# Kernel tuning notes

Measured on AMD Instinct MI355X. Metric: run time of the kernel, lower is better.

## Reference

```python
import jax, jax.numpy as jnp
import numpy as np

B, T, D, H = 64, 512, 512, 1024


def setup_inputs() -> dict:
    key = jax.random.key(0)
    k0, k1, k2, k3, k4 = jax.random.split(key, 5)
    s0 = 1.0 / np.sqrt(D + H)   # torch nn.Linear init bound, layer 0
    s1 = 1.0 / np.sqrt(H + H)   # layer 1
    x = jax.random.normal(k0, (B, T, D), jnp.float32)
    W0 = jax.random.uniform(k1, (4 * H, D + H), jnp.float32, -s0, s0)
    b0 = jax.random.uniform(k2, (4 * H,), jnp.float32, -s0, s0)
    W1 = jax.random.uniform(k3, (4 * H, H + H), jnp.float32, -s1, s1)
    b1 = jax.random.uniform(k4, (4 * H,), jnp.float32, -s1, s1)
    return {"x": x, "W0": W0, "b0": b0, "W1": W1, "b1": b1}


def _lstm_layer(x, W, b):
    # x: (B, T, Din); W: (4H, Din+H); b: (4H,)
    hdim = b.shape[0] // 4
    bsz = x.shape[0]
    h0 = jnp.zeros((bsz, hdim), x.dtype)
    c0 = jnp.zeros((bsz, hdim), x.dtype)

    def step(carry, x_t):
        h, c = carry
        z = jnp.concatenate([x_t, h], axis=-1) @ W.T + b  # (B, 4H)
        i, f, o, g = jnp.split(z, 4, axis=-1)             # torch split order i,f,o,g
        c_next = jax.nn.sigmoid(f) * c + jax.nn.sigmoid(i) * jnp.tanh(g)
        h_next = jax.nn.sigmoid(o) * jnp.tanh(c_next)
        return (h_next, c_next), h_next

    (_, _), hs = jax.lax.scan(step, (h0, c0), jnp.swapaxes(x, 0, 1))
    return jnp.swapaxes(hs, 0, 1)  # (B, T, H)


def reference(x, W0, b0, W1, b1):
    y = _lstm_layer(x, W0, b0)
    y = _lstm_layer(y, W1, b1)
    return y  # last layer output sequence (return_all_layers=False)
```

## Files before the change

### kernel.cpp

```cpp
#include <hip/hip_runtime.h>
#include <hip/hip_bf16.h>

typedef __bf16 bf16x8 __attribute__((ext_vector_type(8)));
typedef float  f32x4  __attribute__((ext_vector_type(4)));

#define MFMA16(a, b, c) __builtin_amdgcn_mfma_f32_16x16x32_bf16((a), (b), (c), 0, 0, 0)

static constexpr int Bz = 64, Tz = 512, Dz = 512, Hz = 1024;
static constexpr int NWG0 = 128;
static constexpr int NWGT = 256;
static constexpr int NJ   = 8;

static constexpr int PXL = 512 + 8;
static constexpr int PHL = 1024 + 8;
static constexpr size_t LDS_BYTES = (size_t)(2 * 32 * PXL + 32 * PHL) * 2;

static constexpr size_t N_W0X = 4096ull * 512;
static constexpr size_t N_W0H = 4096ull * 1024;
static constexpr size_t N_W1  = 4096ull * 2048;
static constexpr size_t N_Y0  = 64ull * 512 * 1024;
static constexpr size_t N_X   = 64ull * 512 * 512;
static constexpr size_t OFF_W0XH = 0;
static constexpr size_t OFF_W0XL = OFF_W0XH + N_W0X;
static constexpr size_t OFF_W0H  = OFF_W0XL + N_W0X;
static constexpr size_t OFF_W1   = OFF_W0H  + N_W0H;
static constexpr size_t OFF_Y0   = OFF_W1   + N_W1;
static constexpr size_t FLAGS_BYTE = (((OFF_Y0 + N_Y0) * 2) + 255) & ~(size_t)255;
static constexpr size_t H1S_BYTE   = FLAGS_BYTE + 4096;
static constexpr size_t WS_NEED    = H1S_BYTE + N_Y0 * 2;
static constexpr size_t XHI_BYTE   = H1S_BYTE + N_Y0 * 2;
static constexpr size_t XLO_BYTE   = XHI_BYTE + N_X * 2;
static constexpr size_t WS_NEED_X  = XLO_BYTE + N_X * 2;

static constexpr int STEP_ELEMS = 65536;

__device__ __forceinline__ float sigm(float x) { return 1.0f / (1.0f + __expf(-x)); }

__device__ __forceinline__ void st_agent_u32(void* p, unsigned v)
{ __hip_atomic_store((unsigned*)p, v, __ATOMIC_RELAXED, __HIP_MEMORY_SCOPE_AGENT); }
__device__ __forceinline__ void st_agent_f32(float* p, float v)
{ __hip_atomic_store(p, v, __ATOMIC_RELAXED, __HIP_MEMORY_SCOPE_AGENT); }

extern "C" __global__ void prep_split(const float* __restrict__ x,
                                      const float* __restrict__ W0,
                                      const float* __restrict__ W1,
                                      __bf16* __restrict__ ws,
                                      __bf16* __restrict__ xhi,
                                      __bf16* __restrict__ xlo)
{
    if (blockIdx.x == 0)
        for (int i = threadIdx.x; i < 1024; i += 256)
            ((unsigned*)((char*)ws + FLAGS_BYTE))[i] = 0u;

    __bf16* w0xh = ws + OFF_W0XH;
    __bf16* w0xl = ws + OFF_W0XL;
    __bf16* w0h  = ws + OFF_W0H;
    __bf16* w1c  = ws + OFF_W1;
    const size_t ntot = N_W0X + N_W0H + N_W1;
    const size_t stride = (size_t)gridDim.x * blockDim.x;
    for (size_t idx = (size_t)blockIdx.x * blockDim.x + threadIdx.x;
         idx < ntot; idx += stride) {
        if (idx < N_W0X) {
            size_t r = idx >> 9, c = idx & 511;
            float w = W0[r * 1536 + c];
            __bf16 hi = (__bf16)w;
            w0xh[idx] = hi;
            w0xl[idx] = (__bf16)(w - (float)hi);
        } else if (idx < N_W0X + N_W0H) {
            size_t i = idx - N_W0X;
            size_t r = i >> 10, c = i & 1023;
            w0h[i] = (__bf16)W0[r * 1536 + 512 + c];
        } else {
            size_t i = idx - N_W0X - N_W0H;
            w1c[i] = (__bf16)W1[i];
        }
    }
    if (xhi) {
        for (size_t idx = (size_t)blockIdx.x * blockDim.x + threadIdx.x;
             idx < N_X; idx += stride) {
            float v = x[idx];
            __bf16 hi = (__bf16)v;
            xhi[idx] = hi;
            xlo[idx] = (__bf16)(v - (float)hi);
        }
    }
}

__device__ __forceinline__ void publish(unsigned* p, unsigned v)
{
    asm volatile("s_waitcnt vmcnt(0)" ::: "memory");
    __hip_atomic_store(p, v, __ATOMIC_RELAXED, __HIP_MEMORY_SCOPE_AGENT);
}

__device__ __forceinline__ void wait_chunk32(const unsigned* flags, int base, unsigned target)
{
    const unsigned* p = flags + base + (threadIdx.x & 31);
    for (;;) {
        unsigned v = __hip_atomic_load(p, __ATOMIC_RELAXED, __HIP_MEMORY_SCOPE_AGENT);
        if (__all(v >= target)) break;
        __builtin_amdgcn_s_sleep(1);
    }
    asm volatile("" ::: "memory");
}

__device__ __forceinline__ void zx_ps(const __bf16* __restrict__ xh,
                                      const __bf16* __restrict__ xl,
    const __bf16* wxh0, const __bf16* wxl0,
    const __bf16* wxh1, const __bf16* wxl1,
    f32x4& zx0, f32x4& zx1)
{
    f32x4 a0 = {0,0,0,0}, a1 = {0,0,0,0};
#pragma unroll 4
    for (int kk = 0; kk < Dz / 32; ++kk) {
        bf16x8 ahi = *(const bf16x8*)(xh + kk * 32);
        bf16x8 alo = *(const bf16x8*)(xl + kk * 32);
        bf16x8 wh0 = *(const bf16x8*)(wxh0 + kk * 32);
        bf16x8 wl0 = *(const bf16x8*)(wxl0 + kk * 32);
        bf16x8 wh1 = *(const bf16x8*)(wxh1 + kk * 32);
        bf16x8 wl1 = *(const bf16x8*)(wxl1 + kk * 32);
        a0 = MFMA16(ahi, wh0, a0); a0 = MFMA16(alo, wh0, a0); a0 = MFMA16(ahi, wl0, a0);
        a1 = MFMA16(ahi, wh1, a1); a1 = MFMA16(alo, wh1, a1); a1 = MFMA16(ahi, wl1, a1);
    }
    zx0 = a0; zx1 = a1;
}

__device__ __forceinline__ void zx_fb(const float* __restrict__ xt,
    const __bf16* wxh0, const __bf16* wxl0,
    const __bf16* wxh1, const __bf16* wxl1,
    f32x4& zx0, f32x4& zx1)
{
    f32x4 a0 = {0,0,0,0}, a1 = {0,0,0,0};
#pragma unroll 4
    for (int kk = 0; kk < Dz / 32; ++kk) {
        f32x4 va = *(const f32x4*)(xt + kk * 32);
        f32x4 vb = *(const f32x4*)(xt + kk * 32 + 4);
        bf16x8 ahi, alo;
#pragma unroll
        for (int e = 0; e < 4; ++e) {
            float v = va[e]; __bf16 h1 = (__bf16)v;
            ahi[e] = h1; alo[e] = (__bf16)(v - (float)h1);
            float w = vb[e]; __bf16 h2 = (__bf16)w;
            ahi[4 + e] = h2; alo[4 + e] = (__bf16)(w - (float)h2);
        }
        bf16x8 wh0 = *(const bf16x8*)(wxh0 + kk * 32);
        bf16x8 wl0 = *(const bf16x8*)(wxl0 + kk * 32);
        bf16x8 wh1 = *(const bf16x8*)(wxh1 + kk * 32);
        bf16x8 wl1 = *(const bf16x8*)(wxl1 + kk * 32);
        a0 = MFMA16(ahi, wh0, a0); a0 = MFMA16(alo, wh0, a0); a0 = MFMA16(ahi, wl0, a0);
        a1 = MFMA16(ahi, wh1, a1); a1 = MFMA16(alo, wh1, a1); a1 = MFMA16(ahi, wl1, a1);
    }
    zx0 = a0; zx1 = a1;
}

template <bool F32OUT>
__device__ __forceinline__ void gates_store(
    f32x4 za, f32x4 zb, float* cs, int lane, int l15, int rowBase,
    unsigned* yline, float* yf32, size_t rowStride)
{
    f32x4 pa, pb;
#pragma unroll
    for (int e = 0; e < 4; ++e) { pa[e] = __shfl_xor(za[e], 8, 64); pb[e] = __shfl_xor(zb[e], 8, 64); }
    const bool hi = (l15 & 8) != 0;
    int p01[2];
#pragma unroll
    for (int k2 = 0; k2 < 2; ++k2) {
        float zi, zf, zo, zg;
        if (hi) { zi = pa[2 + k2]; zf = za[2 + k2]; zo = pb[2 + k2]; zg = zb[2 + k2]; }
        else    { zi = za[k2];     zf = pa[k2];     zo = zb[k2];     zg = pb[k2];     }
        float cn = sigm(zf) * cs[k2] + sigm(zi) * tanhf(zg);
        float hn = sigm(zo) * tanhf(cn);
        cs[k2] = cn;
        if (F32OUT) {
            int b = rowBase + (hi ? 2 : 0) + k2;
            st_agent_f32(&yf32[(size_t)b * rowStride], hn);
        }
        __bf16 hb = (__bf16)hn;
        unsigned bits = (unsigned)__builtin_bit_cast(unsigned short, hb);
        unsigned par  = __shfl_down(bits, 1, 64);
        p01[k2] = (int)(bits | (par << 16));
    }
    if (yline) {
        int r    = lane >> 2;
        int srcl = ((r >> 2) << 4) | (((r >> 1) & 1) << 3) | ((lane & 3) << 1);
        unsigned v0 = (unsigned)__builtin_amdgcn_ds_bpermute(srcl * 4, p01[0]);
        unsigned v1 = (unsigned)__builtin_amdgcn_ds_bpermute(srcl * 4, p01[1]);
        st_agent_u32(yline + lane, (r & 1) ? v1 : v0);
    }
}

__device__ __forceinline__ void layer0(
    const float* __restrict__ x,
    const __bf16* __restrict__ xhi, const __bf16* __restrict__ xlo,
    const __bf16* __restrict__ w0xh, const __bf16* __restrict__ w0xl,
    const __bf16* __restrict__ w0h,  const float* __restrict__ b0,
    __bf16* y0, __bf16* wtile, unsigned* flags0)
{
    const int tid  = threadIdx.x;
    const int wave = tid >> 6, lane = tid & 63, l15 = lane & 15, lg = lane >> 4;
    const int wg   = blockIdx.x;
    const int j0   = wg * NJ;

    __bf16* sWXH = wtile;
    __bf16* sWXL = wtile + 32 * PXL;
    __bf16* sWH  = wtile + 64 * PXL;
    for (int idx = tid; idx < 32 * (Dz / 8); idx += 256) {
        int r = idx >> 6, kc = (idx & 63) * 8;
        size_t grow = (size_t)((r >> 3) * Hz + j0 + (r & 7));
        *(bf16x8*)(sWXH + r * PXL + kc) = *(const bf16x8*)(w0xh + grow * Dz + kc);
        *(bf16x8*)(sWXL + r * PXL + kc) = *(const bf16x8*)(w0xl + grow * Dz + kc);
    }
    for (int idx = tid; idx < 32 * (Hz / 8); idx += 256) {
        int r = idx >> 7, kc = (idx & 127) * 8;
        size_t grow = (size_t)((r >> 3) * Hz + j0 + (r & 7));
        *(bf16x8*)(sWH + r * PHL + kc) = *(const bf16x8*)(w0h + grow * Hz + kc);
    }
    __syncthreads();

    const __bf16* wxh[2]; const __bf16* wxl[2]; const __bf16* whp[2]; float bv[2];
#pragma unroll
    for (int tn = 0; tn < 2; ++tn) {
        int c = tn * 16 + l15;
        wxh[tn] = sWXH + c * PXL + lg * 8;
        wxl[tn] = sWXL + c * PXL + lg * 8;
        whp[tn] = sWH  + c * PHL + lg * 8;
        bv[tn]  = b0[(c >> 3) * Hz + j0 + (c & 7)];
    }
    const int bA = wave * 16 + l15;
    const float*  xp  = x + (size_t)bA * Tz * Dz + lg * 8;
    const __bf16* xph = xhi ? xhi + (size_t)bA * Tz * Dz + lg * 8 : nullptr;
    const __bf16* xpl = xlo ? xlo + (size_t)bA * Tz * Dz + lg * 8 : nullptr;
    const __bf16* hp0 = y0 + wave * 128 + l15 * 8 + lg * 512;

    const unsigned* flw = flags0 + wave * 128;
    unsigned* myflag     = flags0 + wave * 128 + wg;

    float cs[2] = {0.f, 0.f};
    f32x4 zx0, zx1;
    if (xph) zx_ps(xph, xpl, wxh[0], wxl[0], wxh[1], wxl[1], zx0, zx1);
    else     zx_fb(xp,       wxh[0], wxl[0], wxh[1], wxl[1], zx0, zx1);

    for (int s = 0; s < Tz; ++s) {
        f32x4 ah0 = {0,0,0,0}, ah1 = {0,0,0,0};
        if (s > 0) {
            const __bf16* ht = hp0 + (size_t)(s - 1) * STEP_ELEMS;
            for (int c = 0; c < 4; ++c) {
                wait_chunk32(flw, 32 * c, (unsigned)s);
#pragma unroll
                for (int kk = 8 * c; kk < 8 * c + 8; ++kk) {
                    bf16x8 a = *(const bf16x8*)(ht + kk * 2048);
                    ah0 = MFMA16(a, *(const bf16x8*)(whp[0] + kk * 32), ah0);
                    ah1 = MFMA16(a, *(const bf16x8*)(whp[1] + kk * 32), ah1);
                }
            }
        }
        f32x4 za, zb;
#pragma unroll
        for (int e = 0; e < 4; ++e) { za[e] = zx0[e] + ah0[e] + bv[0]; zb[e] = zx1[e] + ah1[e] + bv[1]; }

        unsigned* yline = (unsigned*)y0 + (size_t)s * (STEP_ELEMS / 2) + wg * 256 + wave * 64;
        gates_store<false>(za, zb, cs, lane, l15, wave * 16 + lg * 4, yline, nullptr, 0);

        publish(myflag, (unsigned)(s + 1));
        if (s < Tz - 1) {
            if (xph) zx_ps(xph + (size_t)(s + 1) * Dz, xpl + (size_t)(s + 1) * Dz,
                           wxh[0], wxl[0], wxh[1], wxl[1], zx0, zx1);
            else     zx_fb(xp + (size_t)(s + 1) * Dz,
                           wxh[0], wxl[0], wxh[1], wxl[1], zx0, zx1);
        }
    }
}

__device__ __forceinline__ void layer1(
    const __bf16* __restrict__ y0, const __bf16* __restrict__ w1c,
    const float* __restrict__ b1, float* out, __bf16* h1s,
    __bf16* wtile, unsigned* flags0, unsigned* flags1)
{
    const int tid  = threadIdx.x;
    const int wave = tid >> 6, lane = tid & 63, l15 = lane & 15, lg = lane >> 4;
    const int wg   = blockIdx.x - NWG0;
    const int j0   = wg * NJ;

    __bf16* sWX = wtile;
    __bf16* sWH = wtile + 32 * PHL;
    for (int idx = tid; idx < 32 * (Hz / 8); idx += 256) {
        int r = idx >> 7, kc = (idx & 127) * 8;
        size_t grow = (size_t)((r >> 3) * Hz + j0 + (r & 7));
        const __bf16* srow = w1c + grow * 2048;
        *(bf16x8*)(sWX + r * PHL + kc) = *(const bf16x8*)(srow + kc);
        *(bf16x8*)(sWH + r * PHL + kc) = *(const bf16x8*)(srow + 1024 + kc);
    }
    __syncthreads();

    const __bf16* wxp[2]; const __bf16* whp[2]; float bv[2];
#pragma unroll
    for (int tn = 0; tn < 2; ++tn) {
        int c = tn * 16 + l15;
        wxp[tn] = sWX + c * PHL + lg * 8;
        whp[tn] = sWH + c * PHL + lg * 8;
        bv[tn]  = b1[(c >> 3) * Hz + j0 + (c & 7)];
    }
    const int bA = wave * 16 + l15;
    const __bf16* xp0 = y0 + wave * 128 + l15 * 8 + lg * 512;
    const float*  hpf = out + (size_t)bA * Tz * Hz + lg * 8;
    const __bf16* hs0 = h1s ? h1s + wave * 128 + l15 * 8 + lg * 512 : nullptr;

    const unsigned* fl0w = flags0 + wave * 128;
    const unsigned* fl1w = flags1 + wave * 128;
    unsigned* myflag      = flags1 + wave * 128 + wg;

    float cs[2] = {0.f, 0.f};

    for (int s = 1; s <= Tz; ++s) {
        const int t = s - 1;
        f32x4 ax0 = {bv[0], bv[0], bv[0], bv[0]};
        f32x4 ax1 = {bv[1], bv[1], bv[1], bv[1]};

        if (t > 0) {
            if (hs0) {
                const __bf16* ht = hs0 + (size_t)(t - 1) * STEP_ELEMS;
                for (int c = 0; c < 4; ++c) {
                    wait_chunk32(fl1w, 32 * c, (unsigned)(s - 1));
#pragma unroll
                    for (int kk = 8 * c; kk < 8 * c + 8; ++kk) {
                        bf16x8 a = *(const bf16x8*)(ht + kk * 2048);
                        ax0 = MFMA16(a, *(const bf16x8*)(whp[0] + kk * 32), ax0);
                        ax1 = MFMA16(a, *(const bf16x8*)(whp[1] + kk * 32), ax1);
                    }
                }
            } else {
                const float* ht = hpf + (size_t)(t - 1) * Hz;
                for (int c = 0; c < 4; ++c) {
                    wait_chunk32(fl1w, 32 * c, (unsigned)(s - 1));
#pragma unroll
                    for (int kk = 8 * c; kk < 8 * c + 8; ++kk) {
                        f32x4 va = *(const f32x4*)(ht + kk * 32);
                        f32x4 vb = *(const f32x4*)(ht + kk * 32 + 4);
                        bf16x8 a;
#pragma unroll
                        for (int e = 0; e < 4; ++e) { a[e] = (__bf16)va[e]; a[4 + e] = (__bf16)vb[e]; }
                        ax0 = MFMA16(a, *(const bf16x8*)(whp[0] + kk * 32), ax0);
                        ax1 = MFMA16(a, *(const bf16x8*)(whp[1] + kk * 32), ax1);
                    }
                }
            }
        }
        {
            const __bf16* xt = xp0 + (size_t)t * STEP_ELEMS;
            for (int c = 0; c < 4; ++c) {
                wait_chunk32(fl0w, 32 * c, (unsigned)s);
#pragma unroll
                for (int kk = 8 * c; kk < 8 * c + 8; ++kk) {
                    bf16x8 a = *(const bf16x8*)(xt + kk * 2048);
                    ax0 = MFMA16(a, *(const bf16x8*)(wxp[0] + kk * 32), ax0);
                    ax1 = MFMA16(a, *(const bf16x8*)(wxp[1] + kk * 32), ax1);
                }
            }
        }

        unsigned* hline = h1s ? (unsigned*)h1s + (size_t)t * (STEP_ELEMS / 2) + wg * 256 + wave * 64
                              : nullptr;
        gates_store<true>(ax0, ax1, cs, lane, l15, wave * 16 + lg * 4,
                          hline, out + (size_t)t * Hz + j0 + (l15 & 7), (size_t)Tz * Hz);

        if (s < Tz) publish(myflag, (unsigned)s);
    }
}

extern "C" __global__ void __launch_bounds__(256, 1)
lstm2(const float* __restrict__ x,
      const float* __restrict__ b0,
      const float* __restrict__ b1,
      __bf16* ws,
      float* out,
      __bf16* h1s,
      const __bf16* __restrict__ xhi,
      const __bf16* __restrict__ xlo)
{
    extern __shared__ char lds_raw[];
    __bf16* wtile = (__bf16*)lds_raw;
    unsigned* flags0 = (unsigned*)((char*)ws + FLAGS_BYTE);
    unsigned* flags1 = (unsigned*)((char*)ws + FLAGS_BYTE + 2048);

    if (blockIdx.x < NWG0)
        layer0(x, xhi, xlo, ws + OFF_W0XH, ws + OFF_W0XL, ws + OFF_W0H, b0,
               ws + OFF_Y0, wtile, flags0);
    else
        layer1(ws + OFF_Y0, ws + OFF_W1, b1, out, h1s, wtile, flags0, flags1);
}

extern "C" void kernel_launch(void* const* d_in, const int* in_sizes, int n_in,
                              void* d_out, int out_size, void* d_ws, size_t ws_size,
                              hipStream_t stream)
{
    const float* x  = (const float*)d_in[0];
    const float* W0 = (const float*)d_in[1];
    const float* b0 = (const float*)d_in[2];
    const float* W1 = (const float*)d_in[3];
    const float* b1 = (const float*)d_in[4];
    float* out = (float*)d_out;
    __bf16* ws = (__bf16*)d_ws;
    __bf16* h1s = (ws_size >= WS_NEED)   ? (__bf16*)((char*)ws + H1S_BYTE) : nullptr;
    __bf16* xhi = (ws_size >= WS_NEED_X) ? (__bf16*)((char*)ws + XHI_BYTE) : nullptr;
    __bf16* xlo = (ws_size >= WS_NEED_X) ? (__bf16*)((char*)ws + XLO_BYTE) : nullptr;

    (void)hipFuncSetAttribute((const void*)lstm2,
                        hipFuncAttributeMaxDynamicSharedMemorySize, (int)LDS_BYTES);

    hipLaunchKernelGGL(prep_split, dim3(2048), dim3(256), 0, stream, x, W0, W1, ws, xhi, xlo);

    const __bf16* xhic = xhi; const __bf16* xloc = xlo;
    void* args[] = { (void*)&x, (void*)&b0, (void*)&b1, (void*)&ws, (void*)&out,
                     (void*)&h1s, (void*)&xhic, (void*)&xloc };
    (void)hipLaunchCooperativeKernel(reinterpret_cast<void*>(lstm2),
                               dim3(NWGT), dim3(256), args, LDS_BYTES, stream);
}
```

Baseline: 5.123 ms.

## Split gate columns across two wave groups with LDS exchange of partial gates

Doubles the workgroup to 512 threads so each wave computes one 16-column gate tile instead of two, halving the per-wave MFMA chain in the recurrent step. The second wave group writes its gate pre-activations to LDS and signals through a per-row LDS flag. The first group then combines both tiles, applies the LSTM cell and publishes h. This shortens the serial critical path per timestep. In exchange it adds an intra-block LDS spin handshake and more waves per CU, which raises register pressure.

```diff
diff --git a/kernel.cpp b/kernel.cpp
--- a/kernel.cpp
+++ b/kernel.cpp
@@ -10,10 +10,14 @@
 static constexpr int NWG0 = 128;
 static constexpr int NWGT = 256;
 static constexpr int NJ   = 8;
+static constexpr int NTHR = 512;
 
 static constexpr int PXL = 512 + 8;
 static constexpr int PHL = 1024 + 8;
-static constexpr size_t LDS_BYTES = (size_t)(2 * 32 * PXL + 32 * PHL) * 2;
+static constexpr size_t WT_BYTES  = (size_t)(2 * 32 * PXL + 32 * PHL) * 2;
+static constexpr size_t ZEX_OFF   = WT_BYTES;
+static constexpr size_t ZFLG_OFF  = ZEX_OFF + 4096;
+static constexpr size_t LDS_BYTES = ZFLG_OFF + 16;
 
 static constexpr size_t N_W0X = 4096ull * 512;
 static constexpr size_t N_W0H = 4096ull * 1024;
@@ -103,33 +107,40 @@
     asm volatile("" ::: "memory");
 }
 
-__device__ __forceinline__ void zx_ps(const __bf16* __restrict__ xh,
-                                      const __bf16* __restrict__ xl,
-    const __bf16* wxh0, const __bf16* wxl0,
-    const __bf16* wxh1, const __bf16* wxl1,
-    f32x4& zx0, f32x4& zx1)
-{
-    f32x4 a0 = {0,0,0,0}, a1 = {0,0,0,0};
+__device__ __forceinline__ void zpub(float* dst, f32x4 z, volatile unsigned* f,
+                                     unsigned v, int lane)
+{
+    *(f32x4*)(dst + lane * 4) = z;
+    asm volatile("s_waitcnt lgkmcnt(0)" ::: "memory");
+    if (lane == 0) *f = v;
+}
+__device__ __forceinline__ f32x4 zget(const float* src, volatile const unsigned* f,
+                                      unsigned tgt, int lane)
+{
+    while (*f < tgt) __builtin_amdgcn_s_sleep(1);
+    asm volatile("" ::: "memory");
+    return *(const f32x4*)(src + lane * 4);
+}
+
+__device__ __forceinline__ f32x4 zx1_ps(const __bf16* __restrict__ xh,
+                                        const __bf16* __restrict__ xl,
+                                        const __bf16* wh, const __bf16* wl)
+{
+    f32x4 a = {0, 0, 0, 0};
 #pragma unroll 4
     for (int kk = 0; kk < Dz / 32; ++kk) {
         bf16x8 ahi = *(const bf16x8*)(xh + kk * 32);
         bf16x8 alo = *(const bf16x8*)(xl + kk * 32);
-        bf16x8 wh0 = *(const bf16x8*)(wxh0 + kk * 32);
-        bf16x8 wl0 = *(const bf16x8*)(wxl0 + kk * 32);
-        bf16x8 wh1 = *(const bf16x8*)(wxh1 + kk * 32);
-        bf16x8 wl1 = *(const bf16x8*)(wxl1 + kk * 32);
-        a0 = MFMA16(ahi, wh0, a0); a0 = MFMA16(alo, wh0, a0); a0 = MFMA16(ahi, wl0, a0);
-        a1 = MFMA16(ahi, wh1, a1); a1 = MFMA16(alo, wh1, a1); a1 = MFMA16(ahi, wl1, a1);
-    }
-    zx0 = a0; zx1 = a1;
-}
-
-__device__ __forceinline__ void zx_fb(const float* __restrict__ xt,
-    const __bf16* wxh0, const __bf16* wxl0,
-    const __bf16* wxh1, const __bf16* wxl1,
-    f32x4& zx0, f32x4& zx1)
-{
-    f32x4 a0 = {0,0,0,0}, a1 = {0,0,0,0};
+        bf16x8 w1 = *(const bf16x8*)(wh + kk * 32);
+        bf16x8 w2 = *(const bf16x8*)(wl + kk * 32);
+        a = MFMA16(ahi, w1, a); a = MFMA16(alo, w1, a); a = MFMA16(ahi, w2, a);
+    }
+    return a;
+}
+__device__ __forceinline__ f32x4 zx1_fb(const float* __restrict__ xt,
+                                        const __bf16* wh, const __bf16* wl)
+{
+    f32x4 a = {0, 0, 0, 0};
 #pragma unroll 4
     for (int kk = 0; kk < Dz / 32; ++kk) {
         f32x4 va = *(const f32x4*)(xt + kk * 32);
@@ -142,14 +153,11 @@
             float w = vb[e]; __bf16 h2 = (__bf16)w;
             ahi[4 + e] = h2; alo[4 + e] = (__bf16)(w - (float)h2);
         }
-        bf16x8 wh0 = *(const bf16x8*)(wxh0 + kk * 32);
-        bf16x8 wl0 = *(const bf16x8*)(wxl0 + kk * 32);
-        bf16x8 wh1 = *(const bf16x8*)(wxh1 + kk * 32);
-        bf16x8 wl1 = *(const bf16x8*)(wxl1 + kk * 32);
-        a0 = MFMA16(ahi, wh0, a0); a0 = MFMA16(alo, wh0, a0); a0 = MFMA16(ahi, wl0, a0);
-        a1 = MFMA16(ahi, wh1, a1); a1 = MFMA16(alo, wh1, a1); a1 = MFMA16(ahi, wl1, a1);
-    }
-    zx0 = a0; zx1 = a1;
+        bf16x8 w1 = *(const bf16x8*)(wh + kk * 32);
+        bf16x8 w2 = *(const bf16x8*)(wl + kk * 32);
+        a = MFMA16(ahi, w1, a); a = MFMA16(alo, w1, a); a = MFMA16(ahi, w2, a);
+    }
+    return a;
 }
 
 template <bool F32OUT>
@@ -193,79 +201,77 @@
     const __bf16* __restrict__ xhi, const __bf16* __restrict__ xlo,
     const __bf16* __restrict__ w0xh, const __bf16* __restrict__ w0xl,
     const __bf16* __restrict__ w0h,  const float* __restrict__ b0,
-    __bf16* y0, __bf16* wtile, unsigned* flags0)
+    __bf16* y0, __bf16* wtile, float* zex, volatile unsigned* zflg, unsigned* flags0)
 {
     const int tid  = threadIdx.x;
     const int wave = tid >> 6, lane = tid & 63, l15 = lane & 15, lg = lane >> 4;
-    const int wg   = blockIdx.x;
-    const int j0   = wg * NJ;
+    const int m = wave & 3, n = wave >> 2;
+    const int wg = blockIdx.x, j0 = wg * NJ;
 
     __bf16* sWXH = wtile;
     __bf16* sWXL = wtile + 32 * PXL;
     __bf16* sWH  = wtile + 64 * PXL;
-    for (int idx = tid; idx < 32 * (Dz / 8); idx += 256) {
+    for (int idx = tid; idx < 32 * (Dz / 8); idx += NTHR) {
         int r = idx >> 6, kc = (idx & 63) * 8;
         size_t grow = (size_t)((r >> 3) * Hz + j0 + (r & 7));
         *(bf16x8*)(sWXH + r * PXL + kc) = *(const bf16x8*)(w0xh + grow * Dz + kc);
         *(bf16x8*)(sWXL + r * PXL + kc) = *(const bf16x8*)(w0xl + grow * Dz + kc);
     }
-    for (int idx = tid; idx < 32 * (Hz / 8); idx += 256) {
+    for (int idx = tid; idx < 32 * (Hz / 8); idx += NTHR) {
         int r = idx >> 7, kc = (idx & 127) * 8;
         size_t grow = (size_t)((r >> 3) * Hz + j0 + (r & 7));
         *(bf16x8*)(sWH + r * PHL + kc) = *(const bf16x8*)(w0h + grow * Hz + kc);
     }
+    if (tid < 4) zflg[tid] = 0u;
     __syncthreads();
 
-    const __bf16* wxh[2]; const __bf16* wxl[2]; const __bf16* whp[2]; float bv[2];
-#pragma unroll
-    for (int tn = 0; tn < 2; ++tn) {
-        int c = tn * 16 + l15;
-        wxh[tn] = sWXH + c * PXL + lg * 8;
-        wxl[tn] = sWXL + c * PXL + lg * 8;
-        whp[tn] = sWH  + c * PHL + lg * 8;
-        bv[tn]  = b0[(c >> 3) * Hz + j0 + (c & 7)];
-    }
-    const int bA = wave * 16 + l15;
+    const int c = n * 16 + l15;
+    const __bf16* wxhp = sWXH + c * PXL + lg * 8;
+    const __bf16* wxlp = sWXL + c * PXL + lg * 8;
+    const __bf16* whpp = sWH  + c * PHL + lg * 8;
+    const float bv = b0[(c >> 3) * Hz + j0 + (c & 7)];
+
+    const int bA = m * 16 + l15;
     const float*  xp  = x + (size_t)bA * Tz * Dz + lg * 8;
     const __bf16* xph = xhi ? xhi + (size_t)bA * Tz * Dz + lg * 8 : nullptr;
     const __bf16* xpl = xlo ? xlo + (size_t)bA * Tz * Dz + lg * 8 : nullptr;
-    const __bf16* hp0 = y0 + wave * 128 + l15 * 8 + lg * 512;
-
-    const unsigned* flw = flags0 + wave * 128;
-    unsigned* myflag     = flags0 + wave * 128 + wg;
+    const __bf16* hp0 = y0 + m * 128 + l15 * 8 + lg * 512;
+
+    const unsigned* flw = flags0 + m * 128;
+    unsigned* myflag     = flags0 + m * 128 + wg;
+    float* zexm = zex + m * 256;
 
     float cs[2] = {0.f, 0.f};
-    f32x4 zx0, zx1;
-    if (xph) zx_ps(xph, xpl, wxh[0], wxl[0], wxh[1], wxl[1], zx0, zx1);
-    else     zx_fb(xp,       wxh[0], wxl[0], wxh[1], wxl[1], zx0, zx1);
+    f32x4 zx = xph ? zx1_ps(xph, xpl, wxhp, wxlp) : zx1_fb(xp, wxhp, wxlp);
 
     for (int s = 0; s < Tz; ++s) {
-        f32x4 ah0 = {0,0,0,0}, ah1 = {0,0,0,0};
+        f32x4 ah = {0, 0, 0, 0};
         if (s > 0) {
             const __bf16* ht = hp0 + (size_t)(s - 1) * STEP_ELEMS;
-            for (int c = 0; c < 4; ++c) {
-                wait_chunk32(flw, 32 * c, (unsigned)s);
-#pragma unroll
-                for (int kk = 8 * c; kk < 8 * c + 8; ++kk) {
+            for (int c4 = 0; c4 < 4; ++c4) {
+                wait_chunk32(flw, 32 * c4, (unsigned)s);
+#pragma unroll
+                for (int kk = 8 * c4; kk < 8 * c4 + 8; ++kk) {
                     bf16x8 a = *(const bf16x8*)(ht + kk * 2048);
-                    ah0 = MFMA16(a, *(const bf16x8*)(whp[0] + kk * 32), ah0);
-                    ah1 = MFMA16(a, *(const bf16x8*)(whp[1] + kk * 32), ah1);
+                    ah = MFMA16(a, *(const bf16x8*)(whpp + kk * 32), ah);
                 }
             }
         }
-        f32x4 za, zb;
-#pragma unroll
-        for (int e = 0; e < 4; ++e) { za[e] = zx0[e] + ah0[e] + bv[0]; zb[e] = zx1[e] + ah1[e] + bv[1]; }
-
-        unsigned* yline = (unsigned*)y0 + (size_t)s * (STEP_ELEMS / 2) + wg * 256 + wave * 64;
-        gates_store<false>(za, zb, cs, lane, l15, wave * 16 + lg * 4, yline, nullptr, 0);
-
-        publish(myflag, (unsigned)(s + 1));
+        f32x4 z;
+#pragma unroll
+        for (int e = 0; e < 4; ++e) z[e] = zx[e] + ah[e] + bv;
+
+        if (n == 1) {
+            zpub(zexm, z, &zflg[m], (unsigned)(s + 1), lane);
+        } else {
+            f32x4 zb = zget(zexm, &zflg[m], (unsigned)(s + 1), lane);
+            unsigned* yline = (unsigned*)y0 + (size_t)s * (STEP_ELEMS / 2) + wg * 256 + m * 64;
+            gates_store<false>(z, zb, cs, lane, l15, m * 16 + lg * 4, yline, nullptr, 0);
+            publish(myflag, (unsigned)(s + 1));
+        }
         if (s < Tz - 1) {
-            if (xph) zx_ps(xph + (size_t)(s + 1) * Dz, xpl + (size_t)(s + 1) * Dz,
-                           wxh[0], wxl[0], wxh[1], wxl[1], zx0, zx1);
-            else     zx_fb(xp + (size_t)(s + 1) * Dz,
-                           wxh[0], wxl[0], wxh[1], wxl[1], zx0, zx1);
+            zx = xph ? zx1_ps(xph + (size_t)(s + 1) * Dz, xpl + (size_t)(s + 1) * Dz, wxhp, wxlp)
+                     : zx1_fb(xp + (size_t)(s + 1) * Dz, wxhp, wxlp);
         }
     }
 }
@@ -273,100 +279,100 @@
 __device__ __forceinline__ void layer1(
     const __bf16* __restrict__ y0, const __bf16* __restrict__ w1c,
     const float* __restrict__ b1, float* out, __bf16* h1s,
-    __bf16* wtile, unsigned* flags0, unsigned* flags1)
+    __bf16* wtile, float* zex, volatile unsigned* zflg,
+    unsigned* flags0, unsigned* flags1)
 {
     const int tid  = threadIdx.x;
     const int wave = tid >> 6, lane = tid & 63, l15 = lane & 15, lg = lane >> 4;
-    const int wg   = blockIdx.x - NWG0;
-    const int j0   = wg * NJ;
+    const int m = wave & 3, n = wave >> 2;
+    const int wg = blockIdx.x - NWG0, j0 = wg * NJ;
 
     __bf16* sWX = wtile;
     __bf16* sWH = wtile + 32 * PHL;
-    for (int idx = tid; idx < 32 * (Hz / 8); idx += 256) {
+    for (int idx = tid; idx < 32 * (Hz / 8); idx += NTHR) {
         int r = idx >> 7, kc = (idx & 127) * 8;
         size_t grow = (size_t)((r >> 3) * Hz + j0 + (r & 7));
         const __bf16* srow = w1c + grow * 2048;
         *(bf16x8*)(sWX + r * PHL + kc) = *(const bf16x8*)(srow + kc);
         *(bf16x8*)(sWH + r * PHL + kc) = *(const bf16x8*)(srow + 1024 + kc);
     }
+    if (tid < 4) zflg[tid] = 0u;
     __syncthreads();
 
-    const __bf16* wxp[2]; const __bf16* whp[2]; float bv[2];
-#pragma unroll
-    for (int tn = 0; tn < 2; ++tn) {
-        int c = tn * 16 + l15;
-        wxp[tn] = sWX + c * PHL + lg * 8;
-        whp[tn] = sWH + c * PHL + lg * 8;
-        bv[tn]  = b1[(c >> 3) * Hz + j0 + (c & 7)];
-    }
-    const int bA = wave * 16 + l15;
-    const __bf16* xp0 = y0 + wave * 128 + l15 * 8 + lg * 512;
+    const int c = n * 16 + l15;
+    const __bf16* wxpp = sWX + c * PHL + lg * 8;
+    const __bf16* whpp = sWH + c * PHL + lg * 8;
+    const float bv = b1[(c >> 3) * Hz + j0 + (c & 7)];
+
+    const int bA = m * 16 + l15;
+    const __bf16* xp0 = y0 + m * 128 + l15 * 8 + lg * 512;
     const float*  hpf = out + (size_t)bA * Tz * Hz + lg * 8;
-    const __bf16* hs0 = h1s ? h1s + wave * 128 + l15 * 8 + lg * 512 : nullptr;
-
-    const unsigned* fl0w = flags0 + wave * 128;
-    const unsigned* fl1w = flags1 + wave * 128;
-    unsigned* myflag      = flags1 + wave * 128 + wg;
+    const __bf16* hs0 = h1s ? h1s + m * 128 + l15 * 8 + lg * 512 : nullptr;
+
+    const unsigned* fl0w = flags0 + m * 128;
+    const unsigned* fl1w = flags1 + m * 128;
+    unsigned* myflag      = flags1 + m * 128 + wg;
+    float* zexm = zex + m * 256;
 
     float cs[2] = {0.f, 0.f};
 
     for (int s = 1; s <= Tz; ++s) {
         const int t = s - 1;
-        f32x4 ax0 = {bv[0], bv[0], bv[0], bv[0]};
-        f32x4 ax1 = {bv[1], bv[1], bv[1], bv[1]};
+        f32x4 az = {bv, bv, bv, bv};
 
         if (t > 0) {
             if (hs0) {
                 const __bf16* ht = hs0 + (size_t)(t - 1) * STEP_ELEMS;
-                for (int c = 0; c < 4; ++c) {
-                    wait_chunk32(fl1w, 32 * c, (unsigned)(s - 1));
-#pragma unroll
-                    for (int kk = 8 * c; kk < 8 * c + 8; ++kk) {
+                for (int c4 = 0; c4 < 4; ++c4) {
+                    wait_chunk32(fl1w, 32 * c4, (unsigned)(s - 1));
+#pragma unroll
+                    for (int kk = 8 * c4; kk < 8 * c4 + 8; ++kk) {
                         bf16x8 a = *(const bf16x8*)(ht + kk * 2048);
-                        ax0 = MFMA16(a, *(const bf16x8*)(whp[0] + kk * 32), ax0);
-                        ax1 = MFMA16(a, *(const bf16x8*)(whp[1] + kk * 32), ax1);
+                        az = MFMA16(a, *(const bf16x8*)(whpp + kk * 32), az);
                     }
                 }
             } else {
                 const float* ht = hpf + (size_t)(t - 1) * Hz;
-                for (int c = 0; c < 4; ++c) {
-                    wait_chunk32(fl1w, 32 * c, (unsigned)(s - 1));
-#pragma unroll
-                    for (int kk = 8 * c; kk < 8 * c + 8; ++kk) {
+                for (int c4 = 0; c4 < 4; ++c4) {
+                    wait_chunk32(fl1w, 32 * c4, (unsigned)(s - 1));
+#pragma unroll
+                    for (int kk = 8 * c4; kk < 8 * c4 + 8; ++kk) {
                         f32x4 va = *(const f32x4*)(ht + kk * 32);
                         f32x4 vb = *(const f32x4*)(ht + kk * 32 + 4);
                         bf16x8 a;
 #pragma unroll
                         for (int e = 0; e < 4; ++e) { a[e] = (__bf16)va[e]; a[4 + e] = (__bf16)vb[e]; }
-                        ax0 = MFMA16(a, *(const bf16x8*)(whp[0] + kk * 32), ax0);
-                        ax1 = MFMA16(a, *(const bf16x8*)(whp[1] + kk * 32), ax1);
+                        az = MFMA16(a, *(const bf16x8*)(whpp + kk * 32), az);
                     }
                 }
             }
         }
         {
             const __bf16* xt = xp0 + (size_t)t * STEP_ELEMS;
-            for (int c = 0; c < 4; ++c) {
-                wait_chunk32(fl0w, 32 * c, (unsigned)s);
-#pragma unroll
-                for (int kk = 8 * c; kk < 8 * c + 8; ++kk) {
+            for (int c4 = 0; c4 < 4; ++c4) {
+                wait_chunk32(fl0w, 32 * c4, (unsigned)s);
+#pragma unroll
+                for (int kk = 8 * c4; kk < 8 * c4 + 8; ++kk) {
                     bf16x8 a = *(const bf16x8*)(xt + kk * 2048);
-                    ax0 = MFMA16(a, *(const bf16x8*)(wxp[0] + kk * 32), ax0);
-                    ax1 = MFMA16(a, *(const bf16x8*)(wxp[1] + kk * 32), ax1);
+                    az = MFMA16(a, *(const bf16x8*)(wxpp + kk * 32), az);
                 }
             }
         }
 
-        unsigned* hline = h1s ? (unsigned*)h1s + (size_t)t * (STEP_ELEMS / 2) + wg * 256 + wave * 64
-                              : nullptr;
-        gates_store<true>(ax0, ax1, cs, lane, l15, wave * 16 + lg * 4,
-                          hline, out + (size_t)t * Hz + j0 + (l15 & 7), (size_t)Tz * Hz);
-
-        if (s < Tz) publish(myflag, (unsigned)s);
-    }
-}
-
-extern "C" __global__ void __launch_bounds__(256, 1)
+        if (n == 1) {
+            zpub(zexm, az, &zflg[m], (unsigned)s, lane);
+        } else {
+            f32x4 zb = zget(zexm, &zflg[m], (unsigned)s, lane);
+            unsigned* hline = h1s ? (unsigned*)h1s + (size_t)t * (STEP_ELEMS / 2) + wg * 256 + m * 64
+                                  : nullptr;
+            gates_store<true>(az, zb, cs, lane, l15, m * 16 + lg * 4,
+                              hline, out + (size_t)t * Hz + j0 + (l15 & 7), (size_t)Tz * Hz);
+            if (s < Tz) publish(myflag, (unsigned)s);
+        }
+    }
+}
+
+extern "C" __global__ void __launch_bounds__(512, 1)
 lstm2(const float* __restrict__ x,
       const float* __restrict__ b0,
       const float* __restrict__ b1,
@@ -378,14 +384,16 @@
 {
     extern __shared__ char lds_raw[];
     __bf16* wtile = (__bf16*)lds_raw;
+    float*  zex   = (float*)(lds_raw + ZEX_OFF);
+    volatile unsigned* zflg = (volatile unsigned*)(lds_raw + ZFLG_OFF);
     unsigned* flags0 = (unsigned*)((char*)ws + FLAGS_BYTE);
     unsigned* flags1 = (unsigned*)((char*)ws + FLAGS_BYTE + 2048);
 
     if (blockIdx.x < NWG0)
         layer0(x, xhi, xlo, ws + OFF_W0XH, ws + OFF_W0XL, ws + OFF_W0H, b0,
-               ws + OFF_Y0, wtile, flags0);
+               ws + OFF_Y0, wtile, zex, zflg, flags0);
     else
-        layer1(ws + OFF_Y0, ws + OFF_W1, b1, out, h1s, wtile, flags0, flags1);
+        layer1(ws + OFF_Y0, ws + OFF_W1, b1, out, h1s, wtile, zex, zflg, flags0, flags1);
 }
 
 extern "C" void kernel_launch(void* const* d_in, const int* in_sizes, int n_in,
@@ -412,5 +420,5 @@
     void* args[] = { (void*)&x, (void*)&b0, (void*)&b1, (void*)&ws, (void*)&out,
                      (void*)&h1s, (void*)&xhic, (void*)&xloc };
     (void)hipLaunchCooperativeKernel(reinterpret_cast<void*>(lstm2),
-                               dim3(NWGT), dim3(256), args, LDS_BYTES, stream);
-}
+                               dim3(NWGT), dim3(NTHR), args, LDS_BYTES, stream);
+}
```

Result: slower. 7.251 ms (+41.5%).
